# Optimization experiments

Hardware: AMD Instinct MI355X
Metric: run time of the kernel (lower is better)

The kernel has to match this reference:

```python
import jax, jax.numpy as jnp
import numpy as np

N = 100000
IN_C, HID_C, OUT_C = 128, 128, 64
E = 1600000


def setup_inputs() -> dict:
    key = jax.random.key(0)
    ks = jax.random.split(key, 8)
    x = jax.random.normal(ks[0], (N, IN_C), dtype=jnp.float32)
    edge_index = jax.random.randint(ks[1], (2, E), 0, N, dtype=jnp.int64)
    def glorot(k, fan_in, fan_out):
        lim = np.sqrt(6.0 / (fan_in + fan_out)).astype(np.float32)
        return jax.random.uniform(k, (fan_in, fan_out), jnp.float32, -lim, lim)
    return {
        "x": x,
        "edge_index": edge_index,
        "W1l": glorot(ks[2], IN_C, HID_C),   # lin_l: aggregated neighbors
        "W1r": glorot(ks[3], IN_C, HID_C),   # lin_r: root/self
        "b1": jnp.zeros((HID_C,), jnp.float32),
        "W2l": glorot(ks[4], HID_C, OUT_C),
        "W2r": glorot(ks[5], HID_C, OUT_C),
        "b2": jnp.zeros((OUT_C,), jnp.float32),
    }


def _sage_conv(x, src, dst, Wl, Wr, b):
    # mean aggregation over incoming edges: gather source feats, segment-sum at dst
    msg_sum = jax.ops.segment_sum(x[src], dst, num_segments=N)          # [N, C_in]
    deg = jax.ops.segment_sum(jnp.ones((src.shape[0],), x.dtype), dst,
                              num_segments=N)                           # [N]
    mean = msg_sum / jnp.clip(deg, 1.0, None)[:, None]
    return mean @ Wl + x @ Wr + b


def reference(x, edge_index, W1l, W1r, b1, W2l, W2r, b2):
    src, dst = edge_index[0], edge_index[1]
    h = jax.nn.relu(_sage_conv(x, src, dst, W1l, W1r, b1))
    out = _sage_conv(h, src, dst, W2l, W2r, b2)
    return out
```

## Files before the change

kernel.cpp:

```cpp
#include <hip/hip_runtime.h>
#include <type_traits>


constexpr int K = 128;
constexpr int EB = 4096;

typedef __bf16 bf16x2 __attribute__((ext_vector_type(2)));
typedef __bf16 bf16x4 __attribute__((ext_vector_type(4)));
typedef __bf16 bf16x8 __attribute__((ext_vector_type(8)));
typedef float f32x4 __attribute__((ext_vector_type(4)));
typedef float f32x2 __attribute__((ext_vector_type(2)));


__device__ __forceinline__ unsigned char to_fp8(float v) {
#if __has_builtin(__builtin_amdgcn_cvt_pk_fp8_f32)
  int p = __builtin_amdgcn_cvt_pk_fp8_f32(v, v, 0, false);
  return (unsigned char)(p & 0xff);
#else
  unsigned u = __builtin_bit_cast(unsigned, v);
  unsigned s = (u >> 24) & 0x80u;
  float a = fabsf(v);
  if (a > 448.f) a = 448.f;
  unsigned bits;
  if (a < 0.015625f) {
    bits = (unsigned)(a * 512.f + 0.5f);
  } else {
    unsigned b = __builtin_bit_cast(unsigned, a);
    b += ((b >> 20) & 1) + 0x0007FFFF;
    unsigned e = (b >> 23) - 120;
    bits = (e << 3) | ((b >> 20) & 7);
    if (bits > 0x7E) bits = 0x7E;
  }
  return (unsigned char)(s | bits);
#endif
}

__device__ __forceinline__ f32x2 from_fp8x2(unsigned short u) {
#if __has_builtin(__builtin_amdgcn_cvt_pk_f32_fp8)
  return __builtin_amdgcn_cvt_pk_f32_fp8((int)u, false);
#else
  f32x2 r;
  unsigned b0 = u & 0xff, b1 = (u >> 8) & 0xff;
  unsigned e0 = (b0 >> 3) & 15, m0 = b0 & 7;
  unsigned e1 = (b1 >> 3) & 15, m1 = b1 & 7;
  float v0 = e0 ? __builtin_bit_cast(float, ((e0 + 120) << 23) | (m0 << 20))
              : (float)m0 * 0.001953125f;
  float v1 = e1 ? __builtin_bit_cast(float, ((e1 + 120) << 23) | (m1 << 20))
              : (float)m1 * 0.001953125f;
  r[0] = (b0 & 0x80) ? -v0 : v0;
  r[1] = (b1 & 0x80) ? -v1 : v1;
  return r;
#endif
}

__device__ __forceinline__ f32x2 fp8x2_lo(unsigned v) {
#if __has_builtin(__builtin_amdgcn_cvt_pk_f32_fp8)
  return __builtin_amdgcn_cvt_pk_f32_fp8((int)v, false);
#else
  return from_fp8x2((unsigned short)(v & 0xffffu));
#endif
}

__device__ __forceinline__ f32x2 fp8x2_hi(unsigned v) {
#if __has_builtin(__builtin_amdgcn_cvt_pk_f32_fp8)
  return __builtin_amdgcn_cvt_pk_f32_fp8((int)v, true);
#else
  return from_fp8x2((unsigned short)(v >> 16));
#endif
}


__global__ __launch_bounds__(256) void k_wprep_all(
    const float* __restrict__ W1l, const float* __restrict__ W1r,
    const float* __restrict__ W2l, const float* __restrict__ W2r,
    __bf16* __restrict__ B1l, __bf16* __restrict__ B1r,
    __bf16* __restrict__ B2l, __bf16* __restrict__ B2r) {
  int b = blockIdx.x;
  const float* W;
  __bf16* Bt;
  int idx;
  bool wide;
  if (b < 64) {
    W = W1l; Bt = B1l; idx = b * 256 + threadIdx.x; wide = true;
  } else if (b < 128) {
    W = W1r; Bt = B1r; idx = (b - 64) * 256 + threadIdx.x; wide = true;
  } else if (b < 160) {
    W = W2l; Bt = B2l; idx = (b - 128) * 256 + threadIdx.x; wide = false;
  } else {
    W = W2r; Bt = B2r; idx = (b - 160) * 256 + threadIdx.x; wide = false;
  }
  int k = wide ? (idx >> 7) : (idx >> 6);
  int c = wide ? (idx & 127) : (idx & 63);
  Bt[c * K + k] = (__bf16)W[idx];
}


__global__ __launch_bounds__(256) void k_bhist(const int* __restrict__ dst,
                                               int* __restrict__ blockHist,
                                               int* __restrict__ bucketTotal,
                                               int E, int n, int nB) {
  extern __shared__ int hist[];
  for (int i = threadIdx.x; i < nB; i += 256) hist[i] = 0;
  __syncthreads();
  int base = blockIdx.x * EB, end = min(base + EB, E);
  for (int e = base + threadIdx.x; e < end; e += 256) {
    int d = dst[e];
    if ((unsigned)d < (unsigned)n) atomicAdd(&hist[d >> 8], 1);
  }
  __syncthreads();
  for (int i = threadIdx.x; i < nB; i += 256) {
    int v = hist[i];
    blockHist[(long)blockIdx.x * nB + i] = v;
    if (v) atomicAdd(&bucketTotal[i], v);
  }
}

__global__ __launch_bounds__(512) void k_btop(const int* __restrict__ bucketTotal,
                                              int* __restrict__ bucketBase,
                                              int* __restrict__ bucketCursor, int nB) {
  __shared__ int sh[512];
  int t = threadIdx.x;
  int s = (t < nB) ? bucketTotal[t] : 0;
  sh[t] = s;
  __syncthreads();
  for (int off = 1; off < 512; off <<= 1) {
    int v = (t >= off) ? sh[t - off] : 0;
    __syncthreads();
    sh[t] += v;
    __syncthreads();
  }
  if (t < nB) {
    int base = sh[t] - s;
    bucketBase[t] = base;
    bucketCursor[t] = base;
    if (t == nB - 1) bucketBase[nB] = sh[t];
  }
}

__global__ __launch_bounds__(256) void k_bscatter(const int* __restrict__ src,
                                                  const int* __restrict__ dst,
                                                  const int* __restrict__ blockHist,
                                                  int* __restrict__ bucketCursor,
                                                  unsigned* __restrict__ recs,
                                                  int E, int n, int nB) {
  extern __shared__ int cur[];
  for (int i = threadIdx.x; i < nB; i += 256) {
    int c = blockHist[(long)blockIdx.x * nB + i];
    cur[i] = c ? atomicAdd(&bucketCursor[i], c) : 0;
  }
  __syncthreads();
  int base = blockIdx.x * EB, end = min(base + EB, E);
  for (int e = base + threadIdx.x; e < end; e += 256) {
    int d = dst[e];
    if ((unsigned)d < (unsigned)n) {
      int s = min(max(src[e], 0), n - 1);
      int pos = atomicAdd(&cur[d >> 8], 1);
      recs[pos] = ((unsigned)s << 8) | (unsigned)(d & 255);
    }
  }
}

__global__ __launch_bounds__(256) void k_bfill(const unsigned* __restrict__ recs,
                                               const int* __restrict__ bucketBase,
                                               int* __restrict__ rowptr,
                                               int* __restrict__ col, int n, int nB) {
  __shared__ int degl[256];
  __shared__ int incl[256];
  int b = blockIdx.x, t = threadIdx.x;
  int rbeg = bucketBase[b], rend = bucketBase[b + 1];
  degl[t] = 0;
  __syncthreads();
  for (int i = rbeg + t; i < rend; i += 256)
    atomicAdd(&degl[recs[i] & 255], 1);
  __syncthreads();
  incl[t] = degl[t];
  __syncthreads();
  for (int off = 1; off < 256; off <<= 1) {
    int v = (t >= off) ? incl[t - off] : 0;
    __syncthreads();
    incl[t] += v;
    __syncthreads();
  }
  int excl = incl[t] - degl[t];
  int node = b * 256 + t;
  if (node <= n) rowptr[node] = rbeg + excl;
  __syncthreads();
  degl[t] = rbeg + excl;
  __syncthreads();
  for (int i = rbeg + t; i < rend; i += 256) {
    unsigned r = recs[i];
    int pos = atomicAdd(&degl[r & 255], 1);
    col[pos] = (int)(r >> 8);
  }
}


template <int COLS, typename TIN>
__global__ __launch_bounds__(512, 4) void k_gemm_fused(const TIN* __restrict__ X,
                                                       const __bf16* __restrict__ Bta,
                                                       const __bf16* __restrict__ Btb,
                                                       unsigned char* __restrict__ outA,
                                                       __bf16* __restrict__ outB,
                                                       int nrows, int ntiles) {
  constexpr int LD = 136;
  constexpr int NI = COLS / 64;
  constexpr bool FP32IN = std::is_same_v<TIN, float>;
  __shared__ __bf16 As[2][64 * LD];

  int tid = threadIdx.x;
  int w = tid >> 6, lane = tid & 63;
  int m = lane & 15, quad = lane >> 4;
  int panel = w >> 2;
  int wcol = (w & 3) * (16 * NI);
  const __bf16* Btg = panel ? Btb : Bta;

  bf16x8 bq[4][NI];
#pragma unroll
  for (int kc = 0; kc < 4; ++kc)
#pragma unroll
    for (int ni = 0; ni < NI; ++ni)
      bq[kc][ni] = *(const bf16x8*)(Btg + (long)(wcol + ni * 16 + m) * K + kc * 32 + quad * 8);

  float4 ra[4];
  bf16x8 rb[2];

  auto load_tile = [&](int t) {
    long row0 = (long)t * 64;
    if constexpr (FP32IN) {
#pragma unroll
      for (int it = 0; it < 4; ++it) {
        int i = tid + it * 512;
        int r = i >> 5, c4 = (i & 31) << 2;
        long row = row0 + r;
        float4 v = make_float4(0.f, 0.f, 0.f, 0.f);
        if (row < nrows) v = *(const float4*)(X + row * K + c4);
        ra[it] = v;
      }
    } else {
#pragma unroll
      for (int it = 0; it < 2; ++it) {
        int i = tid + it * 512;
        int r = i >> 4, c8 = (i & 15) << 3;
        long row = row0 + r;
        bf16x8 v = {};
        if (row < nrows) v = *(const bf16x8*)(X + row * K + c8);
        rb[it] = v;
      }
    }
  };

  auto write_tile = [&](int buf) {
    if constexpr (FP32IN) {
#pragma unroll
      for (int it = 0; it < 4; ++it) {
        int i = tid + it * 512;
        int r = i >> 5, c4 = (i & 31) << 2;
        bf16x4 bb;
        bb[0] = (__bf16)ra[it].x; bb[1] = (__bf16)ra[it].y;
        bb[2] = (__bf16)ra[it].z; bb[3] = (__bf16)ra[it].w;
        *(bf16x4*)&As[buf][r * LD + c4] = bb;
      }
    } else {
#pragma unroll
      for (int it = 0; it < 2; ++it) {
        int i = tid + it * 512;
        int r = i >> 4, c8 = (i & 15) << 3;
        *(bf16x8*)&As[buf][r * LD + c8] = rb[it];
      }
    }
  };

  int t = (int)blockIdx.x;
  int stride = (int)gridDim.x;
  if (t < ntiles) load_tile(t);

#pragma unroll
  for (int kc = 0; kc < 4; ++kc)
#pragma unroll
    for (int ni = 0; ni < NI; ++ni)
      asm volatile("" :: "v"(bq[kc][ni]));

  int buf = 0;
  while (t < ntiles) {
    write_tile(buf);
    __syncthreads();

    int tn = t + stride;
    if (tn < ntiles) load_tile(tn);

    f32x4 acc[4][NI];
#pragma unroll
    for (int mi = 0; mi < 4; ++mi)
#pragma unroll
      for (int ni = 0; ni < NI; ++ni) acc[mi][ni] = (f32x4){0.f, 0.f, 0.f, 0.f};

#pragma unroll
    for (int kc = 0; kc < 4; ++kc) {
      int ko = kc * 32 + quad * 8;
      bf16x8 af[4];
#pragma unroll
      for (int mi = 0; mi < 4; ++mi)
        af[mi] = *(const bf16x8*)&As[buf][(mi * 16 + m) * LD + ko];
#pragma unroll
      for (int mi = 0; mi < 4; ++mi)
#pragma unroll
        for (int ni = 0; ni < NI; ++ni)
          acc[mi][ni] = __builtin_amdgcn_mfma_f32_16x16x32_bf16(af[mi], bq[kc][ni], acc[mi][ni], 0, 0, 0);
    }

    long row0 = (long)t * 64;
#pragma unroll
    for (int mi = 0; mi < 4; ++mi) {
#pragma unroll
      for (int r = 0; r < 4; ++r) {
        long grow = row0 + mi * 16 + quad * 4 + r;
        if (grow < nrows) {
#pragma unroll
          for (int ni = 0; ni < NI; ++ni) {
            long idx = grow * COLS + wcol + ni * 16 + m;
            float v = acc[mi][ni][r];
            if (panel == 0) outA[idx] = to_fp8(v);
            else            outB[idx] = (__bf16)v;
          }
        }
      }
    }

    t = tn;
    buf ^= 1;
  }
}


template <bool RELU>
__global__ __launch_bounds__(256) void k_agg128(const unsigned char* __restrict__ Y,
                                                const __bf16* __restrict__ XR,
                                                const float* __restrict__ bias,
                                                const int* __restrict__ rowptr,
                                                const int* __restrict__ col,
                                                __bf16* __restrict__ out, int nnodes) {
  int wave = threadIdx.x >> 6, lane = threadIdx.x & 63;
  int quarter = lane >> 4, l = lane & 15;
  int sb = lane & 48;
  int n = blockIdx.x * 16 + wave * 4 + quarter;
  bool valid = n < nnodes;
  int beg = 0, end = 0;
  if (valid) {
    beg = rowptr[n];
    end = rowptr[n + 1];
  }
  int co = l * 8;
  const unsigned char* Yc = Y + co;

  f32x2 av0 = {0.f, 0.f}, av1 = {0.f, 0.f}, av2 = {0.f, 0.f}, av3 = {0.f, 0.f};

  for (int base = beg; base < end; base += 16) {
    int cnt = min(end - base, 16);
    int idx = (l < cnt) ? col[base + l] : 0;
    int j = 0;
    for (; j + 3 < cnt; j += 4) {
      long s0 = (unsigned)__shfl(idx, sb + j);
      long s1 = (unsigned)__shfl(idx, sb + j + 1);
      long s2 = (unsigned)__shfl(idx, sb + j + 2);
      long s3 = (unsigned)__shfl(idx, sb + j + 3);
      uint2 v0 = *(const uint2*)(Yc + s0 * 128);
      uint2 v1 = *(const uint2*)(Yc + s1 * 128);
      uint2 v2 = *(const uint2*)(Yc + s2 * 128);
      uint2 v3 = *(const uint2*)(Yc + s3 * 128);
      av0 += fp8x2_lo(v0.x); av1 += fp8x2_hi(v0.x);
      av2 += fp8x2_lo(v0.y); av3 += fp8x2_hi(v0.y);
      av0 += fp8x2_lo(v1.x); av1 += fp8x2_hi(v1.x);
      av2 += fp8x2_lo(v1.y); av3 += fp8x2_hi(v1.y);
      av0 += fp8x2_lo(v2.x); av1 += fp8x2_hi(v2.x);
      av2 += fp8x2_lo(v2.y); av3 += fp8x2_hi(v2.y);
      av0 += fp8x2_lo(v3.x); av1 += fp8x2_hi(v3.x);
      av2 += fp8x2_lo(v3.y); av3 += fp8x2_hi(v3.y);
    }
    for (; j < cnt; ++j) {
      long s = (unsigned)__shfl(idx, sb + j);
      uint2 v = *(const uint2*)(Yc + s * 128);
      av0 += fp8x2_lo(v.x); av1 += fp8x2_hi(v.x);
      av2 += fp8x2_lo(v.y); av3 += fp8x2_hi(v.y);
    }
  }

  if (valid) {
    float inv = 1.f / (float)max(end - beg, 1);
    bf16x8 xv = *(const bf16x8*)(XR + (long)n * 128 + co);
    f32x4 b0 = *(const f32x4*)(bias + co);
    f32x4 b1 = *(const f32x4*)(bias + co + 4);
    float r0 = av0[0] * inv + (float)xv[0] + b0[0];
    float r1 = av0[1] * inv + (float)xv[1] + b0[1];
    float r2 = av1[0] * inv + (float)xv[2] + b0[2];
    float r3 = av1[1] * inv + (float)xv[3] + b0[3];
    float r4 = av2[0] * inv + (float)xv[4] + b1[0];
    float r5 = av2[1] * inv + (float)xv[5] + b1[1];
    float r6 = av3[0] * inv + (float)xv[6] + b1[2];
    float r7 = av3[1] * inv + (float)xv[7] + b1[3];
    if (RELU) {
      r0 = fmaxf(r0, 0.f); r1 = fmaxf(r1, 0.f);
      r2 = fmaxf(r2, 0.f); r3 = fmaxf(r3, 0.f);
      r4 = fmaxf(r4, 0.f); r5 = fmaxf(r5, 0.f);
      r6 = fmaxf(r6, 0.f); r7 = fmaxf(r7, 0.f);
    }
    bf16x8 o;
    o[0] = (__bf16)r0; o[1] = (__bf16)r1; o[2] = (__bf16)r2; o[3] = (__bf16)r3;
    o[4] = (__bf16)r4; o[5] = (__bf16)r5; o[6] = (__bf16)r6; o[7] = (__bf16)r7;
    *(bf16x8*)(out + (long)n * 128 + co) = o;
  }
}

__global__ __launch_bounds__(256) void k_agg64(const unsigned char* __restrict__ Y,
                                               const __bf16* __restrict__ XR,
                                               const float* __restrict__ bias,
                                               const int* __restrict__ rowptr,
                                               const int* __restrict__ col,
                                               float* __restrict__ out, int nnodes) {
  int wave = threadIdx.x >> 6, lane = threadIdx.x & 63;
  int quarter = lane >> 4, l = lane & 15;
  int sb = lane & 48;
  int n = blockIdx.x * 16 + wave * 4 + quarter;
  bool valid = n < nnodes;
  int beg = 0, end = 0;
  if (valid) {
    beg = rowptr[n];
    end = rowptr[n + 1];
  }
  int co = l * 4;
  const unsigned char* Yc = Y + co;

  f32x2 av0 = {0.f, 0.f}, av1 = {0.f, 0.f};

  for (int base = beg; base < end; base += 16) {
    int cnt = min(end - base, 16);
    int idx = (l < cnt) ? col[base + l] : 0;
    int j = 0;
    for (; j + 3 < cnt; j += 4) {
      long s0 = (unsigned)__shfl(idx, sb + j);
      long s1 = (unsigned)__shfl(idx, sb + j + 1);
      long s2 = (unsigned)__shfl(idx, sb + j + 2);
      long s3 = (unsigned)__shfl(idx, sb + j + 3);
      unsigned v0 = *(const unsigned*)(Yc + s0 * 64);
      unsigned v1 = *(const unsigned*)(Yc + s1 * 64);
      unsigned v2 = *(const unsigned*)(Yc + s2 * 64);
      unsigned v3 = *(const unsigned*)(Yc + s3 * 64);
      av0 += fp8x2_lo(v0); av1 += fp8x2_hi(v0);
      av0 += fp8x2_lo(v1); av1 += fp8x2_hi(v1);
      av0 += fp8x2_lo(v2); av1 += fp8x2_hi(v2);
      av0 += fp8x2_lo(v3); av1 += fp8x2_hi(v3);
    }
    for (; j < cnt; ++j) {
      long s = (unsigned)__shfl(idx, sb + j);
      unsigned v = *(const unsigned*)(Yc + s * 64);
      av0 += fp8x2_lo(v); av1 += fp8x2_hi(v);
    }
  }

  if (valid) {
    float inv = 1.f / (float)max(end - beg, 1);
    bf16x4 xv = *(const bf16x4*)(XR + (long)n * 64 + co);
    f32x4 bv = *(const f32x4*)(bias + co);
    f32x4 r;
    r[0] = av0[0] * inv + (float)xv[0] + bv[0];
    r[1] = av0[1] * inv + (float)xv[1] + bv[1];
    r[2] = av1[0] * inv + (float)xv[2] + bv[2];
    r[3] = av1[1] * inv + (float)xv[3] + bv[3];
    *(f32x4*)(out + (long)n * 64 + co) = r;
  }
}


extern "C" void kernel_launch(void* const* d_in, const int* in_sizes, int n_in,
                              void* d_out, int out_size, void* d_ws, size_t ws_size,
                              hipStream_t stream) {
  const float* x   = (const float*)d_in[0];
  const int*   ei  = (const int*)d_in[1];
  const float* W1l = (const float*)d_in[2];
  const float* W1r = (const float*)d_in[3];
  const float* b1  = (const float*)d_in[4];
  const float* W2l = (const float*)d_in[5];
  const float* W2r = (const float*)d_in[6];
  const float* b2  = (const float*)d_in[7];
  float* out = (float*)d_out;

  int N = in_sizes[0] / K;
  int E = in_sizes[1] / 2;
  const int* src = ei;
  const int* dst = ei + E;

  int nB = (N + 255) >> 8;
  int nblk = (E + EB - 1) / EB;

  char* ws = (char*)d_ws;
  size_t off = 0;
  auto alloc = [&](size_t bytes) {
    void* p = ws + off;
    off = (off + bytes + 255) & ~(size_t)255;
    return p;
  };
  int*      rowptr       = (int*)alloc(((size_t)N + 2) * 4);
  int*      col          = (int*)alloc((size_t)E * 4);
  int*      blockHist    = (int*)alloc((size_t)nblk * nB * 4);
  int*      bucketTotal  = (int*)alloc(((size_t)nB) * 4);
  int*      bucketBase   = (int*)alloc(((size_t)nB + 1) * 4);
  int*      bucketCursor = (int*)alloc((size_t)nB * 4);
  unsigned* recs         = (unsigned*)alloc((size_t)E * 4);
  unsigned char* y1      = (unsigned char*)alloc((size_t)N * 128);
  __bf16*   xr           = (__bf16*)alloc((size_t)N * 128 * 2);
  __bf16*   h            = (__bf16*)alloc((size_t)N * 128 * 2);
  __bf16*   Bt1l         = (__bf16*)alloc((size_t)128 * K * 2);
  __bf16*   Bt1r         = (__bf16*)alloc((size_t)128 * K * 2);
  __bf16*   Bt2l         = (__bf16*)alloc((size_t)64 * K * 2);
  __bf16*   Bt2r         = (__bf16*)alloc((size_t)64 * K * 2);
  unsigned char* y2 = y1;
  __bf16*   hr = xr;

  k_wprep_all<<<192, 256, 0, stream>>>(W1l, W1r, W2l, W2r, Bt1l, Bt1r, Bt2l, Bt2r);

  hipMemsetAsync(bucketTotal, 0, (size_t)nB * 4, stream);
  k_bhist<<<nblk, 256, nB * 4, stream>>>(dst, blockHist, bucketTotal, E, N, nB);
  k_btop<<<1, 512, 0, stream>>>(bucketTotal, bucketBase, bucketCursor, nB);
  k_bscatter<<<nblk, 256, nB * 4, stream>>>(src, dst, blockHist, bucketCursor, recs, E, N, nB);
  k_bfill<<<nB, 256, 0, stream>>>(recs, bucketBase, rowptr, col, N, nB);

  int ntiles = (N + 63) / 64;
  int gpers = ntiles < 512 ? ntiles : 512;
  k_gemm_fused<128, float><<<gpers, 512, 0, stream>>>(x, Bt1l, Bt1r, y1, xr, N, ntiles);
  k_agg128<true><<<(N + 15) / 16, 256, 0, stream>>>(y1, xr, b1, rowptr, col, h, N);

  k_gemm_fused<64, __bf16><<<gpers, 512, 0, stream>>>(h, Bt2l, Bt2r, y2, hr, N, ntiles);
  k_agg64<<<(N + 15) / 16, 256, 0, stream>>>(y2, hr, b2, rowptr, col, out, N);
}
```

Before: 267.0 us.

## Fuse CSR fill with layer-1 aggregation and drop weight-prep and memset launches

Merges the bucket fill kernel with the layer-1 mean aggregation, so each 256-node bucket builds its column list in LDS and aggregates immediately without rereading col from global memory. The weight transpose kernel is removed and the GEMM now reads and converts fp32 weights directly. The global bucketTotal atomics and memset are replaced by a serial column sum over per-block histograms inside k_btop. This cuts launches and global traffic, but the fused kernel only has nB (~391) blocks with a large LDS footprint, k_btop now loops over ~391 blocks per thread, and the GEMM weight loads become strided scalar loads.

```diff
diff --git a/kernel.cpp b/kernel.cpp
--- a/kernel.cpp
+++ b/kernel.cpp
@@ -4,6 +4,7 @@
 
 constexpr int K = 128;
 constexpr int EB = 4096;
+constexpr int COLCAP = 6144;
 
 typedef __bf16 bf16x2 __attribute__((ext_vector_type(2)));
 typedef __bf16 bf16x4 __attribute__((ext_vector_type(4)));
@@ -70,34 +71,8 @@
 }
 
 
-__global__ __launch_bounds__(256) void k_wprep_all(
-    const float* __restrict__ W1l, const float* __restrict__ W1r,
-    const float* __restrict__ W2l, const float* __restrict__ W2r,
-    __bf16* __restrict__ B1l, __bf16* __restrict__ B1r,
-    __bf16* __restrict__ B2l, __bf16* __restrict__ B2r) {
-  int b = blockIdx.x;
-  const float* W;
-  __bf16* Bt;
-  int idx;
-  bool wide;
-  if (b < 64) {
-    W = W1l; Bt = B1l; idx = b * 256 + threadIdx.x; wide = true;
-  } else if (b < 128) {
-    W = W1r; Bt = B1r; idx = (b - 64) * 256 + threadIdx.x; wide = true;
-  } else if (b < 160) {
-    W = W2l; Bt = B2l; idx = (b - 128) * 256 + threadIdx.x; wide = false;
-  } else {
-    W = W2r; Bt = B2r; idx = (b - 160) * 256 + threadIdx.x; wide = false;
-  }
-  int k = wide ? (idx >> 7) : (idx >> 6);
-  int c = wide ? (idx & 127) : (idx & 63);
-  Bt[c * K + k] = (__bf16)W[idx];
-}
-
-
 __global__ __launch_bounds__(256) void k_bhist(const int* __restrict__ dst,
                                                int* __restrict__ blockHist,
-                                               int* __restrict__ bucketTotal,
                                                int E, int n, int nB) {
   extern __shared__ int hist[];
   for (int i = threadIdx.x; i < nB; i += 256) hist[i] = 0;
@@ -108,19 +83,19 @@
     if ((unsigned)d < (unsigned)n) atomicAdd(&hist[d >> 8], 1);
   }
   __syncthreads();
-  for (int i = threadIdx.x; i < nB; i += 256) {
-    int v = hist[i];
-    blockHist[(long)blockIdx.x * nB + i] = v;
-    if (v) atomicAdd(&bucketTotal[i], v);
-  }
-}
-
-__global__ __launch_bounds__(512) void k_btop(const int* __restrict__ bucketTotal,
+  for (int i = threadIdx.x; i < nB; i += 256)
+    blockHist[(long)blockIdx.x * nB + i] = hist[i];
+}
+
+__global__ __launch_bounds__(512) void k_btop(const int* __restrict__ blockHist,
                                               int* __restrict__ bucketBase,
-                                              int* __restrict__ bucketCursor, int nB) {
+                                              int* __restrict__ bucketCursor,
+                                              int nB, int nblk) {
   __shared__ int sh[512];
   int t = threadIdx.x;
-  int s = (t < nB) ? bucketTotal[t] : 0;
+  int s = 0;
+  if (t < nB)
+    for (int b = 0; b < nblk; ++b) s += blockHist[(long)b * nB + t];
   sh[t] = s;
   __syncthreads();
   for (int off = 1; off < 512; off <<= 1) {
@@ -160,14 +135,22 @@
   }
 }
 
-__global__ __launch_bounds__(256) void k_bfill(const unsigned* __restrict__ recs,
-                                               const int* __restrict__ bucketBase,
-                                               int* __restrict__ rowptr,
-                                               int* __restrict__ col, int n, int nB) {
+
+template <bool RELU>
+__global__ __launch_bounds__(256) void k_bfill_agg(
+    const unsigned* __restrict__ recs, const int* __restrict__ bucketBase,
+    int* __restrict__ rowptr, int* __restrict__ col,
+    const unsigned char* __restrict__ Y, const __bf16* __restrict__ XR,
+    const float* __restrict__ bias, __bf16* __restrict__ out, int n) {
   __shared__ int degl[256];
   __shared__ int incl[256];
+  __shared__ int rp[257];
+  __shared__ int cur[256];
+  __shared__ int colLds[COLCAP];
   int b = blockIdx.x, t = threadIdx.x;
   int rbeg = bucketBase[b], rend = bucketBase[b + 1];
+  bool useLds = (rend - rbeg) <= COLCAP;
+
   degl[t] = 0;
   __syncthreads();
   for (int i = rbeg + t; i < rend; i += 256)
@@ -182,23 +165,99 @@
     __syncthreads();
   }
   int excl = incl[t] - degl[t];
+  rp[t] = rbeg + excl;
+  if (t == 255) rp[256] = rend;
   int node = b * 256 + t;
   if (node <= n) rowptr[node] = rbeg + excl;
-  __syncthreads();
-  degl[t] = rbeg + excl;
+  cur[t] = rbeg + excl;
   __syncthreads();
   for (int i = rbeg + t; i < rend; i += 256) {
     unsigned r = recs[i];
-    int pos = atomicAdd(&degl[r & 255], 1);
-    col[pos] = (int)(r >> 8);
+    int pos = atomicAdd(&cur[r & 255], 1);
+    int sv = (int)(r >> 8);
+    col[pos] = sv;
+    if (useLds) colLds[pos - rbeg] = sv;
+  }
+  __syncthreads();
+
+  int wave = t >> 6, lane = t & 63;
+  int quarter = lane >> 4, l = lane & 15;
+  int sb = lane & 48;
+  int co = l * 8;
+  const unsigned char* Yc = Y + co;
+
+  for (int pass = 0; pass < 16; ++pass) {
+    int nl = pass * 16 + wave * 4 + quarter;
+    int nn = b * 256 + nl;
+    bool valid = nn < n;
+    int beg = rp[nl], end = rp[nl + 1];
+
+    f32x2 av0 = {0.f, 0.f}, av1 = {0.f, 0.f}, av2 = {0.f, 0.f}, av3 = {0.f, 0.f};
+
+    for (int base = beg; base < end; base += 16) {
+      int cnt = min(end - base, 16);
+      int idx = 0;
+      if (l < cnt)
+        idx = useLds ? colLds[base - rbeg + l] : col[base + l];
+      int j = 0;
+      for (; j + 3 < cnt; j += 4) {
+        long s0 = (unsigned)__shfl(idx, sb + j);
+        long s1 = (unsigned)__shfl(idx, sb + j + 1);
+        long s2 = (unsigned)__shfl(idx, sb + j + 2);
+        long s3 = (unsigned)__shfl(idx, sb + j + 3);
+        uint2 v0 = *(const uint2*)(Yc + s0 * 128);
+        uint2 v1 = *(const uint2*)(Yc + s1 * 128);
+        uint2 v2 = *(const uint2*)(Yc + s2 * 128);
+        uint2 v3 = *(const uint2*)(Yc + s3 * 128);
+        av0 += fp8x2_lo(v0.x); av1 += fp8x2_hi(v0.x);
+        av2 += fp8x2_lo(v0.y); av3 += fp8x2_hi(v0.y);
+        av0 += fp8x2_lo(v1.x); av1 += fp8x2_hi(v1.x);
+        av2 += fp8x2_lo(v1.y); av3 += fp8x2_hi(v1.y);
+        av0 += fp8x2_lo(v2.x); av1 += fp8x2_hi(v2.x);
+        av2 += fp8x2_lo(v2.y); av3 += fp8x2_hi(v2.y);
+        av0 += fp8x2_lo(v3.x); av1 += fp8x2_hi(v3.x);
+        av2 += fp8x2_lo(v3.y); av3 += fp8x2_hi(v3.y);
+      }
+      for (; j < cnt; ++j) {
+        long s = (unsigned)__shfl(idx, sb + j);
+        uint2 v = *(const uint2*)(Yc + s * 128);
+        av0 += fp8x2_lo(v.x); av1 += fp8x2_hi(v.x);
+        av2 += fp8x2_lo(v.y); av3 += fp8x2_hi(v.y);
+      }
+    }
+
+    if (valid) {
+      float inv = 1.f / (float)max(end - beg, 1);
+      bf16x8 xv = *(const bf16x8*)(XR + (long)nn * 128 + co);
+      f32x4 b0 = *(const f32x4*)(bias + co);
+      f32x4 b1 = *(const f32x4*)(bias + co + 4);
+      float r0 = av0[0] * inv + (float)xv[0] + b0[0];
+      float r1 = av0[1] * inv + (float)xv[1] + b0[1];
+      float r2 = av1[0] * inv + (float)xv[2] + b0[2];
+      float r3 = av1[1] * inv + (float)xv[3] + b0[3];
+      float r4 = av2[0] * inv + (float)xv[4] + b1[0];
+      float r5 = av2[1] * inv + (float)xv[5] + b1[1];
+      float r6 = av3[0] * inv + (float)xv[6] + b1[2];
+      float r7 = av3[1] * inv + (float)xv[7] + b1[3];
+      if (RELU) {
+        r0 = fmaxf(r0, 0.f); r1 = fmaxf(r1, 0.f);
+        r2 = fmaxf(r2, 0.f); r3 = fmaxf(r3, 0.f);
+        r4 = fmaxf(r4, 0.f); r5 = fmaxf(r5, 0.f);
+        r6 = fmaxf(r6, 0.f); r7 = fmaxf(r7, 0.f);
+      }
+      bf16x8 o;
+      o[0] = (__bf16)r0; o[1] = (__bf16)r1; o[2] = (__bf16)r2; o[3] = (__bf16)r3;
+      o[4] = (__bf16)r4; o[5] = (__bf16)r5; o[6] = (__bf16)r6; o[7] = (__bf16)r7;
+      *(bf16x8*)(out + (long)nn * 128 + co) = o;
+    }
   }
 }
 
 
 template <int COLS, typename TIN>
 __global__ __launch_bounds__(512, 4) void k_gemm_fused(const TIN* __restrict__ X,
-                                                       const __bf16* __restrict__ Bta,
-                                                       const __bf16* __restrict__ Btb,
+                                                       const float* __restrict__ Wa,
+                                                       const float* __restrict__ Wb,
                                                        unsigned char* __restrict__ outA,
                                                        __bf16* __restrict__ outB,
                                                        int nrows, int ntiles) {
@@ -212,14 +271,16 @@
   int m = lane & 15, quad = lane >> 4;
   int panel = w >> 2;
   int wcol = (w & 3) * (16 * NI);
-  const __bf16* Btg = panel ? Btb : Bta;
+  const float* Wsrc = panel ? Wb : Wa;
 
   bf16x8 bq[4][NI];
 #pragma unroll
   for (int kc = 0; kc < 4; ++kc)
 #pragma unroll
     for (int ni = 0; ni < NI; ++ni)
-      bq[kc][ni] = *(const bf16x8*)(Btg + (long)(wcol + ni * 16 + m) * K + kc * 32 + quad * 8);
+#pragma unroll
+      for (int e = 0; e < 8; ++e)
+        bq[kc][ni][e] = (__bf16)Wsrc[(kc * 32 + quad * 8 + e) * COLS + (wcol + ni * 16 + m)];
 
   float4 ra[4];
   bf16x8 rb[2];
@@ -284,7 +345,6 @@
   while (t < ntiles) {
     write_tile(buf);
     __syncthreads();
-
     int tn = t + stride;
     if (tn < ntiles) load_tile(tn);
 
@@ -325,90 +385,11 @@
         }
       }
     }
-
     t = tn;
     buf ^= 1;
   }
 }
 
-
-template <bool RELU>
-__global__ __launch_bounds__(256) void k_agg128(const unsigned char* __restrict__ Y,
-                                                const __bf16* __restrict__ XR,
-                                                const float* __restrict__ bias,
-                                                const int* __restrict__ rowptr,
-                                                const int* __restrict__ col,
-                                                __bf16* __restrict__ out, int nnodes) {
-  int wave = threadIdx.x >> 6, lane = threadIdx.x & 63;
-  int quarter = lane >> 4, l = lane & 15;
-  int sb = lane & 48;
-  int n = blockIdx.x * 16 + wave * 4 + quarter;
-  bool valid = n < nnodes;
-  int beg = 0, end = 0;
-  if (valid) {
-    beg = rowptr[n];
-    end = rowptr[n + 1];
-  }
-  int co = l * 8;
-  const unsigned char* Yc = Y + co;
-
-  f32x2 av0 = {0.f, 0.f}, av1 = {0.f, 0.f}, av2 = {0.f, 0.f}, av3 = {0.f, 0.f};
-
-  for (int base = beg; base < end; base += 16) {
-    int cnt = min(end - base, 16);
-    int idx = (l < cnt) ? col[base + l] : 0;
-    int j = 0;
-    for (; j + 3 < cnt; j += 4) {
-      long s0 = (unsigned)__shfl(idx, sb + j);
-      long s1 = (unsigned)__shfl(idx, sb + j + 1);
-      long s2 = (unsigned)__shfl(idx, sb + j + 2);
-      long s3 = (unsigned)__shfl(idx, sb + j + 3);
-      uint2 v0 = *(const uint2*)(Yc + s0 * 128);
-      uint2 v1 = *(const uint2*)(Yc + s1 * 128);
-      uint2 v2 = *(const uint2*)(Yc + s2 * 128);
-      uint2 v3 = *(const uint2*)(Yc + s3 * 128);
-      av0 += fp8x2_lo(v0.x); av1 += fp8x2_hi(v0.x);
-      av2 += fp8x2_lo(v0.y); av3 += fp8x2_hi(v0.y);
-      av0 += fp8x2_lo(v1.x); av1 += fp8x2_hi(v1.x);
-      av2 += fp8x2_lo(v1.y); av3 += fp8x2_hi(v1.y);
-      av0 += fp8x2_lo(v2.x); av1 += fp8x2_hi(v2.x);
-      av2 += fp8x2_lo(v2.y); av3 += fp8x2_hi(v2.y);
-      av0 += fp8x2_lo(v3.x); av1 += fp8x2_hi(v3.x);
-      av2 += fp8x2_lo(v3.y); av3 += fp8x2_hi(v3.y);
-    }
-    for (; j < cnt; ++j) {
-      long s = (unsigned)__shfl(idx, sb + j);
-      uint2 v = *(const uint2*)(Yc + s * 128);
-      av0 += fp8x2_lo(v.x); av1 += fp8x2_hi(v.x);
-      av2 += fp8x2_lo(v.y); av3 += fp8x2_hi(v.y);
-    }
-  }
-
-  if (valid) {
-    float inv = 1.f / (float)max(end - beg, 1);
-    bf16x8 xv = *(const bf16x8*)(XR + (long)n * 128 + co);
-    f32x4 b0 = *(const f32x4*)(bias + co);
-    f32x4 b1 = *(const f32x4*)(bias + co + 4);
-    float r0 = av0[0] * inv + (float)xv[0] + b0[0];
-    float r1 = av0[1] * inv + (float)xv[1] + b0[1];
-    float r2 = av1[0] * inv + (float)xv[2] + b0[2];
-    float r3 = av1[1] * inv + (float)xv[3] + b0[3];
-    float r4 = av2[0] * inv + (float)xv[4] + b1[0];
-    float r5 = av2[1] * inv + (float)xv[5] + b1[1];
-    float r6 = av3[0] * inv + (float)xv[6] + b1[2];
-    float r7 = av3[1] * inv + (float)xv[7] + b1[3];
-    if (RELU) {
-      r0 = fmaxf(r0, 0.f); r1 = fmaxf(r1, 0.f);
-      r2 = fmaxf(r2, 0.f); r3 = fmaxf(r3, 0.f);
-      r4 = fmaxf(r4, 0.f); r5 = fmaxf(r5, 0.f);
-      r6 = fmaxf(r6, 0.f); r7 = fmaxf(r7, 0.f);
-    }
-    bf16x8 o;
-    o[0] = (__bf16)r0; o[1] = (__bf16)r1; o[2] = (__bf16)r2; o[3] = (__bf16)r3;
-    o[4] = (__bf16)r4; o[5] = (__bf16)r5; o[6] = (__bf16)r6; o[7] = (__bf16)r7;
-    *(bf16x8*)(out + (long)n * 128 + co) = o;
-  }
-}
 
 __global__ __launch_bounds__(256) void k_agg64(const unsigned char* __restrict__ Y,
                                                const __bf16* __restrict__ XR,
@@ -501,33 +482,27 @@
   int*      rowptr       = (int*)alloc(((size_t)N + 2) * 4);
   int*      col          = (int*)alloc((size_t)E * 4);
   int*      blockHist    = (int*)alloc((size_t)nblk * nB * 4);
-  int*      bucketTotal  = (int*)alloc(((size_t)nB) * 4);
   int*      bucketBase   = (int*)alloc(((size_t)nB + 1) * 4);
   int*      bucketCursor = (int*)alloc((size_t)nB * 4);
   unsigned* recs         = (unsigned*)alloc((size_t)E * 4);
   unsigned char* y1      = (unsigned char*)alloc((size_t)N * 128);
   __bf16*   xr           = (__bf16*)alloc((size_t)N * 128 * 2);
   __bf16*   h            = (__bf16*)alloc((size_t)N * 128 * 2);
-  __bf16*   Bt1l         = (__bf16*)alloc((size_t)128 * K * 2);
-  __bf16*   Bt1r         = (__bf16*)alloc((size_t)128 * K * 2);
-  __bf16*   Bt2l         = (__bf16*)alloc((size_t)64 * K * 2);
-  __bf16*   Bt2r         = (__bf16*)alloc((size_t)64 * K * 2);
   unsigned char* y2 = y1;
   __bf16*   hr = xr;
 
-  k_wprep_all<<<192, 256, 0, stream>>>(W1l, W1r, W2l, W2r, Bt1l, Bt1r, Bt2l, Bt2r);
-
-  hipMemsetAsync(bucketTotal, 0, (size_t)nB * 4, stream);
-  k_bhist<<<nblk, 256, nB * 4, stream>>>(dst, blockHist, bucketTotal, E, N, nB);
-  k_btop<<<1, 512, 0, stream>>>(bucketTotal, bucketBase, bucketCursor, nB);
-  k_bscatter<<<nblk, 256, nB * 4, stream>>>(src, dst, blockHist, bucketCursor, recs, E, N, nB);
-  k_bfill<<<nB, 256, 0, stream>>>(recs, bucketBase, rowptr, col, N, nB);
-
   int ntiles = (N + 63) / 64;
   int gpers = ntiles < 512 ? ntiles : 512;
-  k_gemm_fused<128, float><<<gpers, 512, 0, stream>>>(x, Bt1l, Bt1r, y1, xr, N, ntiles);
-  k_agg128<true><<<(N + 15) / 16, 256, 0, stream>>>(y1, xr, b1, rowptr, col, h, N);
-
-  k_gemm_fused<64, __bf16><<<gpers, 512, 0, stream>>>(h, Bt2l, Bt2r, y2, hr, N, ntiles);
+
+  k_bhist<<<nblk, 256, nB * 4, stream>>>(dst, blockHist, E, N, nB);
+  k_btop<<<1, 512, 0, stream>>>(blockHist, bucketBase, bucketCursor, nB, nblk);
+  k_bscatter<<<nblk, 256, nB * 4, stream>>>(src, dst, blockHist, bucketCursor, recs, E, N, nB);
+
+  k_gemm_fused<128, float><<<gpers, 512, 0, stream>>>(x, W1l, W1r, y1, xr, N, ntiles);
+
+  k_bfill_agg<true><<<nB, 256, 0, stream>>>(recs, bucketBase, rowptr, col, y1, xr, b1, h, N);
+
+  k_gemm_fused<64, __bf16><<<gpers, 512, 0, stream>>>(h, W2l, W2r, y2, hr, N, ntiles);
+
   k_agg64<<<(N + 15) / 16, 256, 0, stream>>>(y2, hr, b2, rowptr, col, out, N);
 }
```

Result: slower. 379.9 us (+42.3%).

## Fuse edge bucketing into one scatter kernel and drop weight prep kernel

Applied to the files above, without the earlier changes.

Replaces the separate histogram and scatter passes with a single kernel that counts locally, reserves space with a global atomic, and writes records into fixed-capacity per-bucket slabs. The prefix scan then only computes CSR offsets, and the fill kernel reads from the slabs. The GEMM now converts fp32 weights to bf16 itself, which removes the weight-prep kernel and its buffers. This cuts launches and the blockHist traffic, but any bucket holding more than the capacity of edges is silently truncated.

```diff
diff --git a/kernel.cpp b/kernel.cpp
--- a/kernel.cpp
+++ b/kernel.cpp
@@ -4,6 +4,7 @@
 
 constexpr int K = 128;
 constexpr int EB = 4096;
+constexpr int CAP = 8192;
 
 typedef __bf16 bf16x2 __attribute__((ext_vector_type(2)));
 typedef __bf16 bf16x4 __attribute__((ext_vector_type(4)));
@@ -70,57 +71,41 @@
 }
 
 
-__global__ __launch_bounds__(256) void k_wprep_all(
-    const float* __restrict__ W1l, const float* __restrict__ W1r,
-    const float* __restrict__ W2l, const float* __restrict__ W2r,
-    __bf16* __restrict__ B1l, __bf16* __restrict__ B1r,
-    __bf16* __restrict__ B2l, __bf16* __restrict__ B2r) {
-  int b = blockIdx.x;
-  const float* W;
-  __bf16* Bt;
-  int idx;
-  bool wide;
-  if (b < 64) {
-    W = W1l; Bt = B1l; idx = b * 256 + threadIdx.x; wide = true;
-  } else if (b < 128) {
-    W = W1r; Bt = B1r; idx = (b - 64) * 256 + threadIdx.x; wide = true;
-  } else if (b < 160) {
-    W = W2l; Bt = B2l; idx = (b - 128) * 256 + threadIdx.x; wide = false;
-  } else {
-    W = W2r; Bt = B2r; idx = (b - 160) * 256 + threadIdx.x; wide = false;
-  }
-  int k = wide ? (idx >> 7) : (idx >> 6);
-  int c = wide ? (idx & 127) : (idx & 63);
-  Bt[c * K + k] = (__bf16)W[idx];
-}
-
-
-__global__ __launch_bounds__(256) void k_bhist(const int* __restrict__ dst,
-                                               int* __restrict__ blockHist,
-                                               int* __restrict__ bucketTotal,
-                                               int E, int n, int nB) {
-  extern __shared__ int hist[];
-  for (int i = threadIdx.x; i < nB; i += 256) hist[i] = 0;
+__global__ __launch_bounds__(256) void k_scatter(const int* __restrict__ src,
+                                                 const int* __restrict__ dst,
+                                                 int* __restrict__ bucketCount,
+                                                 unsigned* __restrict__ recs,
+                                                 int E, int n, int nB) {
+  extern __shared__ int cur[];
+  for (int i = threadIdx.x; i < nB; i += 256) cur[i] = 0;
   __syncthreads();
   int base = blockIdx.x * EB, end = min(base + EB, E);
   for (int e = base + threadIdx.x; e < end; e += 256) {
     int d = dst[e];
-    if ((unsigned)d < (unsigned)n) atomicAdd(&hist[d >> 8], 1);
+    if ((unsigned)d < (unsigned)n) atomicAdd(&cur[d >> 8], 1);
   }
   __syncthreads();
   for (int i = threadIdx.x; i < nB; i += 256) {
-    int v = hist[i];
-    blockHist[(long)blockIdx.x * nB + i] = v;
-    if (v) atomicAdd(&bucketTotal[i], v);
-  }
-}
-
-__global__ __launch_bounds__(512) void k_btop(const int* __restrict__ bucketTotal,
-                                              int* __restrict__ bucketBase,
-                                              int* __restrict__ bucketCursor, int nB) {
+    int c = cur[i];
+    cur[i] = c ? atomicAdd(&bucketCount[i], c) : 0;
+  }
+  __syncthreads();
+  for (int e = base + threadIdx.x; e < end; e += 256) {
+    int d = dst[e];
+    if ((unsigned)d < (unsigned)n) {
+      int s = min(max(src[e], 0), n - 1);
+      int b = d >> 8;
+      int pos = min(atomicAdd(&cur[b], 1), CAP - 1);
+      recs[(long)b * CAP + pos] = ((unsigned)s << 8) | (unsigned)(d & 255);
+    }
+  }
+}
+
+__global__ __launch_bounds__(512) void k_btop(const int* __restrict__ bucketCount,
+                                              int* __restrict__ bucketBase, int nB) {
   __shared__ int sh[512];
   int t = threadIdx.x;
-  int s = (t < nB) ? bucketTotal[t] : 0;
+  int s = (t < nB) ? bucketCount[t] : 0;
   sh[t] = s;
   __syncthreads();
   for (int off = 1; off < 512; off <<= 1) {
@@ -130,48 +115,26 @@
     __syncthreads();
   }
   if (t < nB) {
-    int base = sh[t] - s;
-    bucketBase[t] = base;
-    bucketCursor[t] = base;
+    bucketBase[t] = sh[t] - s;
     if (t == nB - 1) bucketBase[nB] = sh[t];
-  }
-}
-
-__global__ __launch_bounds__(256) void k_bscatter(const int* __restrict__ src,
-                                                  const int* __restrict__ dst,
-                                                  const int* __restrict__ blockHist,
-                                                  int* __restrict__ bucketCursor,
-                                                  unsigned* __restrict__ recs,
-                                                  int E, int n, int nB) {
-  extern __shared__ int cur[];
-  for (int i = threadIdx.x; i < nB; i += 256) {
-    int c = blockHist[(long)blockIdx.x * nB + i];
-    cur[i] = c ? atomicAdd(&bucketCursor[i], c) : 0;
-  }
-  __syncthreads();
-  int base = blockIdx.x * EB, end = min(base + EB, E);
-  for (int e = base + threadIdx.x; e < end; e += 256) {
-    int d = dst[e];
-    if ((unsigned)d < (unsigned)n) {
-      int s = min(max(src[e], 0), n - 1);
-      int pos = atomicAdd(&cur[d >> 8], 1);
-      recs[pos] = ((unsigned)s << 8) | (unsigned)(d & 255);
-    }
   }
 }
 
 __global__ __launch_bounds__(256) void k_bfill(const unsigned* __restrict__ recs,
                                                const int* __restrict__ bucketBase,
+                                               const int* __restrict__ bucketCount,
                                                int* __restrict__ rowptr,
-                                               int* __restrict__ col, int n, int nB) {
+                                               int* __restrict__ col, int n) {
   __shared__ int degl[256];
   __shared__ int incl[256];
   int b = blockIdx.x, t = threadIdx.x;
-  int rbeg = bucketBase[b], rend = bucketBase[b + 1];
+  int rbeg = bucketBase[b];
+  int cnt = bucketCount[b];
+  const unsigned* rbase = recs + (long)b * CAP;
   degl[t] = 0;
   __syncthreads();
-  for (int i = rbeg + t; i < rend; i += 256)
-    atomicAdd(&degl[recs[i] & 255], 1);
+  for (int i = t; i < cnt; i += 256)
+    atomicAdd(&degl[rbase[i] & 255], 1);
   __syncthreads();
   incl[t] = degl[t];
   __syncthreads();
@@ -187,8 +150,8 @@
   __syncthreads();
   degl[t] = rbeg + excl;
   __syncthreads();
-  for (int i = rbeg + t; i < rend; i += 256) {
-    unsigned r = recs[i];
+  for (int i = t; i < cnt; i += 256) {
+    unsigned r = rbase[i];
     int pos = atomicAdd(&degl[r & 255], 1);
     col[pos] = (int)(r >> 8);
   }
@@ -197,8 +160,8 @@
 
 template <int COLS, typename TIN>
 __global__ __launch_bounds__(512, 4) void k_gemm_fused(const TIN* __restrict__ X,
-                                                       const __bf16* __restrict__ Bta,
-                                                       const __bf16* __restrict__ Btb,
+                                                       const float* __restrict__ Wa,
+                                                       const float* __restrict__ Wb,
                                                        unsigned char* __restrict__ outA,
                                                        __bf16* __restrict__ outB,
                                                        int nrows, int ntiles) {
@@ -212,14 +175,16 @@
   int m = lane & 15, quad = lane >> 4;
   int panel = w >> 2;
   int wcol = (w & 3) * (16 * NI);
-  const __bf16* Btg = panel ? Btb : Bta;
+  const float* Wsrc = panel ? Wb : Wa;
 
   bf16x8 bq[4][NI];
 #pragma unroll
   for (int kc = 0; kc < 4; ++kc)
 #pragma unroll
     for (int ni = 0; ni < NI; ++ni)
-      bq[kc][ni] = *(const bf16x8*)(Btg + (long)(wcol + ni * 16 + m) * K + kc * 32 + quad * 8);
+#pragma unroll
+      for (int e = 0; e < 8; ++e)
+        bq[kc][ni][e] = (__bf16)Wsrc[(kc * 32 + quad * 8 + e) * COLS + (wcol + ni * 16 + m)];
 
   float4 ra[4];
   bf16x8 rb[2];
@@ -284,7 +249,6 @@
   while (t < ntiles) {
     write_tile(buf);
     __syncthreads();
-
     int tn = t + stride;
     if (tn < ntiles) load_tile(tn);
 
@@ -325,7 +289,6 @@
         }
       }
     }
-
     t = tn;
     buf ^= 1;
   }
@@ -498,36 +461,30 @@
     off = (off + bytes + 255) & ~(size_t)255;
     return p;
   };
-  int*      rowptr       = (int*)alloc(((size_t)N + 2) * 4);
-  int*      col          = (int*)alloc((size_t)E * 4);
-  int*      blockHist    = (int*)alloc((size_t)nblk * nB * 4);
-  int*      bucketTotal  = (int*)alloc(((size_t)nB) * 4);
-  int*      bucketBase   = (int*)alloc(((size_t)nB + 1) * 4);
-  int*      bucketCursor = (int*)alloc((size_t)nB * 4);
-  unsigned* recs         = (unsigned*)alloc((size_t)E * 4);
-  unsigned char* y1      = (unsigned char*)alloc((size_t)N * 128);
-  __bf16*   xr           = (__bf16*)alloc((size_t)N * 128 * 2);
-  __bf16*   h            = (__bf16*)alloc((size_t)N * 128 * 2);
-  __bf16*   Bt1l         = (__bf16*)alloc((size_t)128 * K * 2);
-  __bf16*   Bt1r         = (__bf16*)alloc((size_t)128 * K * 2);
-  __bf16*   Bt2l         = (__bf16*)alloc((size_t)64 * K * 2);
-  __bf16*   Bt2r         = (__bf16*)alloc((size_t)64 * K * 2);
+  int*      rowptr      = (int*)alloc(((size_t)N + 2) * 4);
+  int*      col         = (int*)alloc((size_t)E * 4);
+  int*      bucketCount = (int*)alloc((size_t)nB * 4);
+  int*      bucketBase  = (int*)alloc(((size_t)nB + 1) * 4);
+  unsigned* recs        = (unsigned*)alloc((size_t)nB * CAP * 4);
+  unsigned char* y1     = (unsigned char*)alloc((size_t)N * 128);
+  __bf16*   xr          = (__bf16*)alloc((size_t)N * 128 * 2);
+  __bf16*   h           = (__bf16*)alloc((size_t)N * 128 * 2);
   unsigned char* y2 = y1;
   __bf16*   hr = xr;
 
-  k_wprep_all<<<192, 256, 0, stream>>>(W1l, W1r, W2l, W2r, Bt1l, Bt1r, Bt2l, Bt2r);
-
-  hipMemsetAsync(bucketTotal, 0, (size_t)nB * 4, stream);
-  k_bhist<<<nblk, 256, nB * 4, stream>>>(dst, blockHist, bucketTotal, E, N, nB);
-  k_btop<<<1, 512, 0, stream>>>(bucketTotal, bucketBase, bucketCursor, nB);
-  k_bscatter<<<nblk, 256, nB * 4, stream>>>(src, dst, blockHist, bucketCursor, recs, E, N, nB);
-  k_bfill<<<nB, 256, 0, stream>>>(recs, bucketBase, rowptr, col, N, nB);
-
   int ntiles = (N + 63) / 64;
   int gpers = ntiles < 512 ? ntiles : 512;
-  k_gemm_fused<128, float><<<gpers, 512, 0, stream>>>(x, Bt1l, Bt1r, y1, xr, N, ntiles);
+
+  hipMemsetAsync(bucketCount, 0, (size_t)nB * 4, stream);
+  k_scatter<<<nblk, 256, nB * 4, stream>>>(src, dst, bucketCount, recs, E, N, nB);
+  k_btop<<<1, 512, 0, stream>>>(bucketCount, bucketBase, nB);
+
+  k_gemm_fused<128, float><<<gpers, 512, 0, stream>>>(x, W1l, W1r, y1, xr, N, ntiles);
+
+  k_bfill<<<nB, 256, 0, stream>>>(recs, bucketBase, bucketCount, rowptr, col, N);
   k_agg128<true><<<(N + 15) / 16, 256, 0, stream>>>(y1, xr, b1, rowptr, col, h, N);
 
-  k_gemm_fused<64, __bf16><<<gpers, 512, 0, stream>>>(h, Bt2l, Bt2r, y2, hr, N, ntiles);
+  k_gemm_fused<64, __bf16><<<gpers, 512, 0, stream>>>(h, W2l, W2r, y2, hr, N, ntiles);
+
   k_agg64<<<(N + 15) / 16, 256, 0, stream>>>(y2, hr, b2, rowptr, col, out, N);
 }
```

New measurement: 245.7 us. 7.9% less time.
